# Performance work log

Measured on AMD Instinct MI355X. Metric: run time of the kernel, lower is better.

The kernel has to match this reference:

```python
import jax, jax.numpy as jnp
import numpy as np

D_DIST = 1.5       # init kwarg d_dist
NUM_LABELS = 64    # K; labels drawn from [0, K), all present w.h.p. at N=200k
B, C, N = 8, 32, 200000


def setup_inputs() -> dict:
    key = jax.random.key(0)
    k1, k2 = jax.random.split(key)
    prediction = jax.random.normal(k1, (B, C, N), dtype=jnp.float32)
    label = jax.random.randint(k2, (B, N), 0, NUM_LABELS)
    return {"prediction": prediction, "label": label}


def _batch_loss(pred, lab):
    # pred: [C, N], lab: [N] int in [0, K)
    K = NUM_LABELS
    counts = jax.ops.segment_sum(jnp.ones(lab.shape, pred.dtype), lab, num_segments=K)  # [K]
    sums = jax.ops.segment_sum(pred.T, lab, num_segments=K)                              # [K, C]
    center = sums / jnp.maximum(counts, 1.0)[:, None]                                    # [K, C] per-label mean
    # square_distance_single(center, center): pairwise sq-dist between the C columns
    # of center (coordinates are the K cluster axes) -> [C, C], exactly as the torch code.
    gram = center.T @ center                       # [C, C]
    n2 = jnp.sum(center * center, axis=0)          # [C]
    sq = jax.nn.relu(n2[:, None] + n2[None, :] - 2.0 * gram)
    # safe sqrt: identical forward to sqrt(relu(sq)) but finite grads at 0
    dist = jnp.where(sq > 0, jnp.sqrt(jnp.where(sq > 0, sq, 1.0)), 0.0)
    hinge = jax.nn.relu(2.0 * D_DIST - dist)
    return jnp.sum(hinge * hinge) / (2.0 * K * (K - 1.0 + 1e-16))


def reference(prediction, label):
    # sum over batches, matching the python loop accumulation
    return jnp.sum(jax.vmap(_batch_loss)(prediction, label))
```

## Files before the change

### kernel.cpp

```cpp
#include <hip/hip_runtime.h>
#include <stdint.h>

#define BATCH   8
#define CDIM    32
#define KLBL    64
#define NPB     200000
#define SLABS   6250
#define CHUNKS  128
#define REC     (KLBL * CDIM + KLBL)

typedef __attribute__((ext_vector_type(8))) short bf16x8;
typedef __attribute__((ext_vector_type(4))) float f32x4;

union ABits { uint32_t u[4]; bf16x8 v; };

__device__ __forceinline__ uint32_t cvtpk_bf16(float lo, float hi) {
  uint32_t r;
  asm volatile("v_cvt_pk_bf16_f32 %0, %1, %2" : "=v"(r) : "v"(lo), "v"(hi));
  return r;
}

__global__ __launch_bounds__(256, 4) void seg_mfma_kernel(
    const float* __restrict__ pred,
    const int*   __restrict__ label,
    float* __restrict__ gsums,
    float* __restrict__ gcounts,
    float* __restrict__ out) {
  __shared__ float s_part[4][REC];

  const int tid = threadIdx.x;
  const int wv = tid >> 6;
  const int ln = tid & 63;
  const int chunk = blockIdx.x, b = blockIdx.y;

  if (chunk == 0 && b == 0 && tid == 0) out[0] = 0.f;

  const int s0 = (int)((long long)chunk * SLABS / CHUNKS);
  const int s1 = (int)((long long)(chunk + 1) * SLABS / CHUNKS);
  const int w0 = s0 + (int)((long long)(s1 - s0) * wv / 4);
  const int w1 = s0 + (int)((long long)(s1 - s0) * (wv + 1) / 4);

  const int crow = ln & 15;
  const int g    = ln >> 4;
  const int kseg = g * 8;

  const float* row0 = pred + ((size_t)b * CDIM + crow) * NPB;
  const float* row1 = pred + ((size_t)b * CDIM + crow + 16) * NPB;
  const int*   labp = label + (size_t)b * NPB;

  f32x4 acc[4][2];
#pragma unroll
  for (int kt = 0; kt < 4; ++kt) {
    acc[kt][0] = (f32x4){0.f, 0.f, 0.f, 0.f};
    acc[kt][1] = (f32x4){0.f, 0.f, 0.f, 0.f};
  }
  uint32_t cnt0 = 0, cnt1 = 0, cnt2 = 0, cnt3 = 0;

  float4 fA0, fA1, fA2, fA3;  int4 lA0, lA1;
  float4 fB0, fB1, fB2, fB3;  int4 lB0, lB1;

  auto loadA = [&](int s) {
    const int n0 = s * 32 + kseg;
    fA0 = *(const float4*)(row0 + n0);
    fA1 = *(const float4*)(row0 + n0 + 4);
    fA2 = *(const float4*)(row1 + n0);
    fA3 = *(const float4*)(row1 + n0 + 4);
    lA0 = *(const int4*)(labp + n0);
    lA1 = *(const int4*)(labp + n0 + 4);
  };
  auto loadB = [&](int s) {
    const int n0 = s * 32 + kseg;
    fB0 = *(const float4*)(row0 + n0);
    fB1 = *(const float4*)(row0 + n0 + 4);
    fB2 = *(const float4*)(row1 + n0);
    fB3 = *(const float4*)(row1 + n0 + 4);
    lB0 = *(const int4*)(labp + n0);
    lB1 = *(const int4*)(labp + n0 + 4);
  };

  ABits b0v, b1v, av[4];

  auto derive = [&](const float4& f0, const float4& f1, const float4& f2,
                    const float4& f3, const int4& l0, const int4& l1) {
    b0v.u[0] = cvtpk_bf16(f0.x, f0.y);
    b0v.u[1] = cvtpk_bf16(f0.z, f0.w);
    b0v.u[2] = cvtpk_bf16(f1.x, f1.y);
    b0v.u[3] = cvtpk_bf16(f1.z, f1.w);
    b1v.u[0] = cvtpk_bf16(f2.x, f2.y);
    b1v.u[1] = cvtpk_bf16(f2.z, f2.w);
    b1v.u[2] = cvtpk_bf16(f3.x, f3.y);
    b1v.u[3] = cvtpk_bf16(f3.z, f3.w);
#pragma unroll
    for (int kt = 0; kt < 4; ++kt) {
      const int tgt = kt * 16 + crow;
      av[kt].u[0] = (l0.x == tgt ? 0x3F80u : 0u) | (l0.y == tgt ? 0x3F800000u : 0u);
      av[kt].u[1] = (l0.z == tgt ? 0x3F80u : 0u) | (l0.w == tgt ? 0x3F800000u : 0u);
      av[kt].u[2] = (l1.x == tgt ? 0x3F80u : 0u) | (l1.y == tgt ? 0x3F800000u : 0u);
      av[kt].u[3] = (l1.z == tgt ? 0x3F80u : 0u) | (l1.w == tgt ? 0x3F800000u : 0u);
      const uint32_t m =
          (uint32_t)(l0.x == tgt) + (uint32_t)(l0.y == tgt) +
          (uint32_t)(l0.z == tgt) + (uint32_t)(l0.w == tgt) +
          (uint32_t)(l1.x == tgt) + (uint32_t)(l1.y == tgt) +
          (uint32_t)(l1.z == tgt) + (uint32_t)(l1.w == tgt);
      if (kt == 0) cnt0 += m; else if (kt == 1) cnt1 += m;
      else if (kt == 2) cnt2 += m; else cnt3 += m;
    }
  };

  auto mfma_step = [&]() {
#pragma unroll
    for (int kt = 0; kt < 4; ++kt) {
      acc[kt][0] = __builtin_amdgcn_mfma_f32_16x16x32_bf16(av[kt].v, b0v.v, acc[kt][0], 0, 0, 0);
      acc[kt][1] = __builtin_amdgcn_mfma_f32_16x16x32_bf16(av[kt].v, b1v.v, acc[kt][1], 0, 0, 0);
    }
  };

  if (w0 < w1) loadA(w0);
  if (w0 + 1 < w1) loadB(w0 + 1);

  int s = w0;
  while (s < w1) {
    derive(fA0, fA1, fA2, fA3, lA0, lA1);
    if (s + 2 < w1) loadA(s + 2);
    __builtin_amdgcn_sched_barrier(0);
    mfma_step();
    ++s;
    if (s >= w1) break;
    derive(fB0, fB1, fB2, fB3, lB0, lB1);
    if (s + 2 < w1) loadB(s + 2);
    __builtin_amdgcn_sched_barrier(0);
    mfma_step();
    ++s;
  }

  s_part[wv][KLBL * CDIM + ln] = 0.f;
#pragma unroll
  for (int kt = 0; kt < 4; ++kt) {
#pragma unroll
    for (int r = 0; r < 4; ++r) {
      const int k = kt * 16 + g * 4 + r;
      s_part[wv][k * CDIM + crow]      = acc[kt][0][r];
      s_part[wv][k * CDIM + 16 + crow] = acc[kt][1][r];
    }
  }
  atomicAdd(&s_part[wv][KLBL * CDIM + 0 * 16 + crow], (float)cnt0);
  atomicAdd(&s_part[wv][KLBL * CDIM + 1 * 16 + crow], (float)cnt1);
  atomicAdd(&s_part[wv][KLBL * CDIM + 2 * 16 + crow], (float)cnt2);
  atomicAdd(&s_part[wv][KLBL * CDIM + 3 * 16 + crow], (float)cnt3);
  __syncthreads();

  float* gs = gsums + (size_t)b * KLBL * CDIM;
  for (int i = tid; i < REC; i += 256) {
    const float v = s_part[0][i] + s_part[1][i] + s_part[2][i] + s_part[3][i];
    if (i < KLBL * CDIM) atomicAdd(&gs[i], v);
    else                 atomicAdd(&gcounts[b * KLBL + (i - KLBL * CDIM)], v);
  }
}

__global__ __launch_bounds__(256) void loss_kernel(
    const float* __restrict__ gsums,
    const float* __restrict__ gcounts,
    float* __restrict__ out) {
  const int b = blockIdx.x;
  __shared__ float s_center[KLBL * CDIM];
  __shared__ float s_red[256];

  for (int i = threadIdx.x; i < KLBL * CDIM; i += 256) {
    const float cnt = fmaxf(gcounts[b * KLBL + (i >> 5)], 1.0f);
    s_center[i] = gsums[(size_t)b * KLBL * CDIM + i] / cnt;
  }
  __syncthreads();

  float acc = 0.f;
  for (int p = threadIdx.x; p < CDIM * CDIM; p += 256) {
    const int i = p >> 5, j = p & 31;
    float gr = 0.f, ni = 0.f, nj = 0.f;
#pragma unroll
    for (int k = 0; k < KLBL; ++k) {
      const float ci = s_center[k * CDIM + i];
      const float cj = s_center[k * CDIM + j];
      gr += ci * cj;
      ni += ci * ci;
      nj += cj * cj;
    }
    float sq = fmaxf(ni + nj - 2.f * gr, 0.f);
    const float dist = (sq > 0.f) ? sqrtf(sq) : 0.f;
    const float h = fmaxf(3.0f - dist, 0.f);
    acc += h * h;
  }

  s_red[threadIdx.x] = acc;
  __syncthreads();
  for (int s = 128; s > 0; s >>= 1) {
    if (threadIdx.x < s) s_red[threadIdx.x] += s_red[threadIdx.x + s];
    __syncthreads();
  }
  if (threadIdx.x == 0)
    atomicAdd(out, s_red[0] / (2.0f * (float)KLBL * ((float)KLBL - 1.0f)));
}

extern "C" void kernel_launch(void* const* d_in, const int* in_sizes, int n_in,
                              void* d_out, int out_size, void* d_ws, size_t ws_size,
                              hipStream_t stream) {
  const float* pred  = (const float*)d_in[0];
  const int*   label = (const int*)d_in[1];
  float* out = (float*)d_out;

  float* gsums   = (float*)d_ws;
  float* gcounts = gsums + (size_t)BATCH * KLBL * CDIM;

  const size_t accum_bytes =
      (size_t)(BATCH * KLBL * CDIM + BATCH * KLBL) * sizeof(float);
  hipMemsetAsync(d_ws, 0, accum_bytes, stream);

  dim3 grid1(CHUNKS, BATCH);
  seg_mfma_kernel<<<grid1, 256, 0, stream>>>(pred, label, gsums, gcounts, out);
  loss_kernel<<<BATCH, 256, 0, stream>>>(gsums, gcounts, out);
}
```

Baseline: 59.84 us.

## Fuse loss computation into segment kernel via last-block-done counter

Removes the separate loss kernel launch. Each block increments a per-batch atomic counter after pushing its partial sums, and the last block for a batch reads the accumulated sums with agent-scope loads and computes that batch's hinge loss. The output zeroing moves from the kernel to a host memset. This saves one kernel launch and its gap, at the cost of an extra memset and a serialized tail executed by one block per batch.

```diff
diff --git a/kernel.cpp b/kernel.cpp
--- a/kernel.cpp
+++ b/kernel.cpp
@@ -19,21 +19,24 @@
   asm volatile("v_cvt_pk_bf16_f32 %0, %1, %2" : "=v"(r) : "v"(lo), "v"(hi));
   return r;
 }
+__device__ __forceinline__ float agent_ld(const float* p) {
+  return __hip_atomic_load(p, __ATOMIC_RELAXED, __HIP_MEMORY_SCOPE_AGENT);
+}
 
 __global__ __launch_bounds__(256, 4) void seg_mfma_kernel(
     const float* __restrict__ pred,
     const int*   __restrict__ label,
     float* __restrict__ gsums,
     float* __restrict__ gcounts,
+    uint32_t* __restrict__ counters,
     float* __restrict__ out) {
   __shared__ float s_part[4][REC];
+  __shared__ uint32_t s_last;
 
   const int tid = threadIdx.x;
   const int wv = tid >> 6;
   const int ln = tid & 63;
   const int chunk = blockIdx.x, b = blockIdx.y;
-
-  if (chunk == 0 && b == 0 && tid == 0) out[0] = 0.f;
 
   const int s0 = (int)((long long)chunk * SLABS / CHUNKS);
   const int s1 = (int)((long long)(chunk + 1) * SLABS / CHUNKS);
@@ -155,30 +158,34 @@
     if (i < KLBL * CDIM) atomicAdd(&gs[i], v);
     else                 atomicAdd(&gcounts[b * KLBL + (i - KLBL * CDIM)], v);
   }
-}
-
-__global__ __launch_bounds__(256) void loss_kernel(
-    const float* __restrict__ gsums,
-    const float* __restrict__ gcounts,
-    float* __restrict__ out) {
-  const int b = blockIdx.x;
-  __shared__ float s_center[KLBL * CDIM];
-  __shared__ float s_red[256];
-
-  for (int i = threadIdx.x; i < KLBL * CDIM; i += 256) {
-    const float cnt = fmaxf(gcounts[b * KLBL + (i >> 5)], 1.0f);
-    s_center[i] = gsums[(size_t)b * KLBL * CDIM + i] / cnt;
-  }
-  __syncthreads();
-
-  float acc = 0.f;
-  for (int p = threadIdx.x; p < CDIM * CDIM; p += 256) {
+
+  __syncthreads();
+  if (tid == 0) {
+    __threadfence();
+    s_last = (__hip_atomic_fetch_add(&counters[b], 1u, __ATOMIC_ACQ_REL,
+                                     __HIP_MEMORY_SCOPE_AGENT) == CHUNKS - 1);
+  }
+  __syncthreads();
+  if (!s_last) return;
+  __threadfence();
+
+  float* cen = &s_part[0][0];
+  float* red = cen + 2048;
+  float* cb  = red + 256;
+  if (tid < 64) cb[tid] = fmaxf(agent_ld(gcounts + b * 64 + tid), 1.0f);
+  __syncthreads();
+  for (int i = tid; i < 2048; i += 256)
+    cen[i] = agent_ld(gsums + (size_t)b * 2048 + i) / cb[i >> 5];
+  __syncthreads();
+
+  float a2 = 0.f;
+  for (int p = tid; p < 1024; p += 256) {
     const int i = p >> 5, j = p & 31;
     float gr = 0.f, ni = 0.f, nj = 0.f;
 #pragma unroll
     for (int k = 0; k < KLBL; ++k) {
-      const float ci = s_center[k * CDIM + i];
-      const float cj = s_center[k * CDIM + j];
+      const float ci = cen[k * 32 + i];
+      const float cj = cen[k * 32 + j];
       gr += ci * cj;
       ni += ci * ci;
       nj += cj * cj;
@@ -186,17 +193,16 @@
     float sq = fmaxf(ni + nj - 2.f * gr, 0.f);
     const float dist = (sq > 0.f) ? sqrtf(sq) : 0.f;
     const float h = fmaxf(3.0f - dist, 0.f);
-    acc += h * h;
-  }
-
-  s_red[threadIdx.x] = acc;
-  __syncthreads();
-  for (int s = 128; s > 0; s >>= 1) {
-    if (threadIdx.x < s) s_red[threadIdx.x] += s_red[threadIdx.x + s];
+    a2 += h * h;
+  }
+  red[tid] = a2;
+  __syncthreads();
+  for (int s2 = 128; s2 > 0; s2 >>= 1) {
+    if (tid < s2) red[tid] += red[tid + s2];
     __syncthreads();
   }
-  if (threadIdx.x == 0)
-    atomicAdd(out, s_red[0] / (2.0f * (float)KLBL * ((float)KLBL - 1.0f)));
+  if (tid == 0)
+    atomicAdd(out, red[0] / (2.0f * (float)KLBL * ((float)KLBL - 1.0f)));
 }
 
 extern "C" void kernel_launch(void* const* d_in, const int* in_sizes, int n_in,
@@ -204,16 +210,17 @@
                               hipStream_t stream) {
   const float* pred  = (const float*)d_in[0];
   const int*   label = (const int*)d_in[1];
-  float* out = (float*)d_out;
-
-  float* gsums   = (float*)d_ws;
-  float* gcounts = gsums + (size_t)BATCH * KLBL * CDIM;
-
-  const size_t accum_bytes =
-      (size_t)(BATCH * KLBL * CDIM + BATCH * KLBL) * sizeof(float);
-  hipMemsetAsync(d_ws, 0, accum_bytes, stream);
+
+  float*    gsums    = (float*)d_ws;
+  float*    gcounts  = gsums + (size_t)BATCH * KLBL * CDIM;
+  uint32_t* counters = (uint32_t*)(gcounts + BATCH * KLBL);
+
+  const size_t zero_bytes =
+      (size_t)(BATCH * KLBL * CDIM + BATCH * KLBL + BATCH) * 4;
+  hipMemsetAsync(d_ws, 0, zero_bytes, stream);
+  hipMemsetAsync(d_out, 0, sizeof(float), stream);
 
   dim3 grid1(CHUNKS, BATCH);
-  seg_mfma_kernel<<<grid1, 256, 0, stream>>>(pred, label, gsums, gcounts, out);
-  loss_kernel<<<BATCH, 256, 0, stream>>>(gsums, gcounts, out);
-}
+  seg_mfma_kernel<<<grid1, 256, 0, stream>>>(pred, label, gsums, gcounts,
+                                             counters, (float*)d_out);
+}
```

Result: slower. 126.3 us (+111.1%).
